# Kernel optimization log

Measured on AMD Instinct MI355X. Metric: run time of the kernel, lower is better.

The kernel has to match this reference:

```python
import jax, jax.numpy as jnp
import numpy as np
from jax import lax

SEQ, BATCH, INPUT, HIDDEN = 2048, 32, 256, 256


def setup_inputs() -> dict:
    key = jax.random.key(0)
    k1, k2, k3 = jax.random.split(key, 3)
    scale = 1.0 / np.sqrt(HIDDEN)
    return {
        "input": jax.random.normal(k1, (SEQ, BATCH, INPUT), dtype=jnp.float32),
        "W_ih": jax.random.normal(k2, (3 * HIDDEN, INPUT), dtype=jnp.float32) * scale,
        "W_hh": jax.random.normal(k3, (3 * HIDDEN, HIDDEN), dtype=jnp.float32) * scale,
        "b_ih": jnp.zeros((3 * HIDDEN,), dtype=jnp.float32),
        "b_hh": jnp.zeros((3 * HIDDEN,), dtype=jnp.float32),
    }


def reference(input, W_ih, W_hh, b_ih, b_hh):
    """Single-layer unidirectional CustomGRU forward.

    Faithful to the torch module, including its quirk: the n-gate gets the
    W_hh_n @ h contribution twice (once un-gated via `gates`, once gated by r).
    Returns (output [S,B,H], h_n [1,B,H]).
    """
    H = W_hh.shape[0] // 3
    W_hn = W_hh[2 * H:]  # [H, H]
    # Precompute input projections for all timesteps (same math, batched GEMM).
    x_proj = jnp.einsum('sbi,gi->sbg', input, W_ih) + b_ih + b_hh  # [S,B,3H]

    def step(h, xp):
        gates = xp + h @ W_hh.T  # [B, 3H]
        r, z, n = jnp.split(gates, 3, axis=1)
        r = jax.nn.sigmoid(r)
        z = jax.nn.sigmoid(z)
        n = jnp.tanh(n + r * (h @ W_hn.T))
        h_new = (1.0 - z) * n + z * h
        return h_new, h_new

    h0 = jnp.zeros((input.shape[1], H), dtype=input.dtype)
    h_last, output = lax.scan(step, h0, x_proj)
    return output, h_last[None, :, :]
```

## Files before the change

### kernel.cpp

```cpp
#include <hip/hip_runtime.h>
#include <stdint.h>
#include <stddef.h>

#define S_LEN 2048
#define BATCH 32
#define NIN   256
#define NH    256
#define NG    768
#define GRUB  32
#define XPB   2048

typedef _Float16 half2_t __attribute__((ext_vector_type(2)));
typedef _Float16 half8_t __attribute__((ext_vector_type(8)));
typedef int      int16v  __attribute__((ext_vector_type(16)));
typedef int      int4v   __attribute__((ext_vector_type(4)));

#if __has_builtin(__builtin_amdgcn_exp2f)
#define EXP2F(x) __builtin_amdgcn_exp2f(x)
#else
#define EXP2F(x) exp2f(x)
#endif

static __device__ __forceinline__ float fdot2(half2_t a, half2_t b, float c) {
  return __builtin_amdgcn_fdot2(a, b, c, false);
}
static __device__ __forceinline__ half2_t pack2(float lo, float hi) {
  half2_t r; r[0] = (_Float16)lo; r[1] = (_Float16)hi; return r;
}
static __device__ __forceinline__ float sigmoid_fast(float x) {
  float e = EXP2F(-1.44269504088896340736f * x);
  return 1.0f / (1.0f + e);
}
static __device__ __forceinline__ float tanh_fast(float x) {
  float e = EXP2F(2.88539008177792681472f * x);
  return 1.0f - 2.0f / (1.0f + e);
}
static __device__ __forceinline__ float dpp_xor1(float v) {
  return __builtin_bit_cast(float,
    __builtin_amdgcn_mov_dpp(__builtin_bit_cast(int, v), 0xB1, 0xF, 0xF, true));
}
static __device__ __forceinline__ float dpp_xor2(float v) {
  return __builtin_bit_cast(float,
    __builtin_amdgcn_mov_dpp(__builtin_bit_cast(int, v), 0x4E, 0xF, 0xF, true));
}

static __device__ __forceinline__ int flags_all12(const int* p) {
  int4v a, b, c;
  asm volatile("global_load_dwordx4 %0, %3, off sc0 sc1\n"
               "global_load_dwordx4 %1, %4, off sc0 sc1\n"
               "global_load_dwordx4 %2, %5, off sc0 sc1\n"
               "s_waitcnt vmcnt(0)"
               : "=v"(a), "=v"(b), "=v"(c)
               : "v"(p), "v"(p + 4), "v"(p + 8)
               : "memory");
  int all = a.x & a.y & a.z & a.w;
  all &= b.x & b.y & b.z & b.w;
  all &= c.x & c.y & c.z & c.w;
  return all;
}
#define FLAGWAIT(BASEP) do {                                                  \
    while (!flags_all12(BASEP)) __builtin_amdgcn_s_sleep(16);                 \
  } while (0)

#define BH(x)    __builtin_bit_cast(half2_t, (x))
#define BW(W, e) __builtin_bit_cast(half2_t, (int)((W)[e]))

#define DOT6(q, U0, U1, U2, U3, U4, U5, o) do {                               \
    a0 = fdot2(BW(U0,(o)+0), BH(q.x), a0); a1 = fdot2(BW(U1,(o)+0), BH(q.x), a1);\
    a2 = fdot2(BW(U2,(o)+0), BH(q.x), a2); a3 = fdot2(BW(U3,(o)+0), BH(q.x), a3);\
    a4 = fdot2(BW(U4,(o)+0), BH(q.x), a4); a5 = fdot2(BW(U5,(o)+0), BH(q.x), a5);\
    a0 = fdot2(BW(U0,(o)+1), BH(q.y), a0); a1 = fdot2(BW(U1,(o)+1), BH(q.y), a1);\
    a2 = fdot2(BW(U2,(o)+1), BH(q.y), a2); a3 = fdot2(BW(U3,(o)+1), BH(q.y), a3);\
    a4 = fdot2(BW(U4,(o)+1), BH(q.y), a4); a5 = fdot2(BW(U5,(o)+1), BH(q.y), a5);\
    a0 = fdot2(BW(U0,(o)+2), BH(q.z), a0); a1 = fdot2(BW(U1,(o)+2), BH(q.z), a1);\
    a2 = fdot2(BW(U2,(o)+2), BH(q.z), a2); a3 = fdot2(BW(U3,(o)+2), BH(q.z), a3);\
    a4 = fdot2(BW(U4,(o)+2), BH(q.z), a4); a5 = fdot2(BW(U5,(o)+2), BH(q.z), a5);\
    a0 = fdot2(BW(U0,(o)+3), BH(q.w), a0); a1 = fdot2(BW(U1,(o)+3), BH(q.w), a1);\
    a2 = fdot2(BW(U2,(o)+3), BH(q.w), a2); a3 = fdot2(BW(U3,(o)+3), BH(q.w), a3);\
    a4 = fdot2(BW(U4,(o)+3), BH(q.w), a4); a5 = fdot2(BW(U5,(o)+3), BH(q.w), a5);\
  } while (0)

#define LDW(W, o) do {                                                        \
    int4 q0 = wsrc[(o) + 0], q1 = wsrc[(o) + 1];                              \
    int4 q2 = wsrc[(o) + 2], q3 = wsrc[(o) + 3];                              \
    W = (int16v){q0.x, q0.y, q0.z, q0.w, q1.x, q1.y, q1.z, q1.w,              \
                 q2.x, q2.y, q2.z, q2.w, q3.x, q3.y, q3.z, q3.w};             \
  } while (0)

#define LOADPIN_W(SRC) \
  int16v W0a, W0b, W1a, W1b, W2a, W2b, W3a, W3b, W4a, W4b, W5a, W5b;         \
  {                                                                           \
    const int4* wsrc = (const int4*)(SRC);                                    \
    LDW(W0a, 0);  LDW(W0b, 4);  LDW(W1a, 8);  LDW(W1b, 12);                   \
    LDW(W2a, 16); LDW(W2b, 20); LDW(W3a, 24); LDW(W3b, 28);                   \
    LDW(W4a, 32); LDW(W4b, 36); LDW(W5a, 40); LDW(W5b, 44);                   \
  }                                                                           \
  asm volatile("" : "+v"(W0a), "+v"(W0b), "+v"(W1a), "+v"(W1b),               \
                    "+v"(W2a), "+v"(W2b), "+v"(W3a), "+v"(W3b),               \
                    "+v"(W4a), "+v"(W4b), "+v"(W5a), "+v"(W5b));

#define DOT6x8() do {                                                         \
    DOT6(q0, W0a, W1a, W2a, W3a, W4a, W5a, 0);                                \
    DOT6(q1, W0a, W1a, W2a, W3a, W4a, W5a, 4);                                \
    DOT6(q2, W0a, W1a, W2a, W3a, W4a, W5a, 8);                                \
    DOT6(q3, W0a, W1a, W2a, W3a, W4a, W5a, 12);                               \
    DOT6(q4, W0b, W1b, W2b, W3b, W4b, W5b, 0);                                \
    DOT6(q5, W0b, W1b, W2b, W3b, W4b, W5b, 4);                                \
    DOT6(q6, W0b, W1b, W2b, W3b, W4b, W5b, 8);                                \
    DOT6(q7, W0b, W1b, W2b, W3b, W4b, W5b, 12);                               \
  } while (0)

#define QREDUCE(MVR, MVZ, MVN) do {                                           \
    float b0 = a0 + dpp_xor1(a0), b1 = a1 + dpp_xor1(a1);                     \
    float b2 = a2 + dpp_xor1(a2), b3 = a3 + dpp_xor1(a3);                     \
    float b4 = a4 + dpp_xor1(a4), b5 = a5 + dpp_xor1(a5);                     \
    float xr_ = jj ? b1 : b0, xz_ = jj ? b3 : b2, xn_ = jj ? b5 : b4;         \
    MVR = xr_ + dpp_xor2(xr_);                                                \
    MVZ = xz_ + dpp_xor2(xz_);                                                \
    MVN = xn_ + dpp_xor2(xn_);                                                \
  } while (0)

__global__ __launch_bounds__(256) void prep_in_kernel(const float* __restrict__ in,
                                                      _Float16* __restrict__ in16,
                                                      int* __restrict__ flags) {
  size_t v = (size_t)blockIdx.x * 256 + threadIdx.x;
  if (blockIdx.x < 9) {
    int i = blockIdx.x * 256 + threadIdx.x;
    if (i < XPB) flags[i] = 0;
    else if (i < XPB + 8) flags[i] = 1;
  }
  const float4* p4 = (const float4*)in;
  float4 a = p4[v * 2 + 0];
  float4 b = p4[v * 2 + 1];
  half8_t o;
  o[0] = (_Float16)a.x; o[1] = (_Float16)a.y; o[2] = (_Float16)a.z; o[3] = (_Float16)a.w;
  o[4] = (_Float16)b.x; o[5] = (_Float16)b.y; o[6] = (_Float16)b.z; o[7] = (_Float16)b.w;
  ((half8_t*)in16)[v] = o;
}

__global__ __launch_bounds__(256) void prep_w_kernel(const float* __restrict__ W_ih,
                                                     const float* __restrict__ W_hh,
                                                     const float* __restrict__ b_ih,
                                                     const float* __restrict__ b_hh,
                                                     half2_t* __restrict__ whh3,
                                                     half2_t* __restrict__ wih3,
                                                     float* __restrict__ bias) {
  int idx = blockIdx.x * 256 + threadIdx.x;
  if (idx < 128 * NG) {
    int tid = idx / 192;
    int r   = idx - tid * 192;
    int d   = r >> 5, kk = r & 31;
    int gate = d >> 1, jj = d & 1;
    int c  = tid & 3, j1 = tid >> 2;
    int row = gate * NH + 2 * j1 + jj;
    int col = 64 * c + 2 * kk;
    whh3[idx] = pack2(W_hh[(size_t)row * NH + col], W_hh[(size_t)row * NH + col + 1]);
  } else if (idx < 2 * 128 * NG) {
    int i2  = idx - 128 * NG;
    int tid = i2 / 192;
    int r   = i2 - tid * 192;
    int d   = r >> 5, kk = r & 31;
    int gate = d >> 1, jj = d & 1;
    int c  = tid & 3, j1 = tid >> 2;
    int row = gate * NH + 2 * j1 + jj;
    int col = 64 * c + 2 * kk;
    wih3[i2] = pack2(W_ih[(size_t)row * NIN + col], W_ih[(size_t)row * NIN + col + 1]);
  } else if (idx < 2 * 128 * NG + NG) {
    int g = idx - 2 * 128 * NG;
    bias[g] = b_ih[g] + b_hh[g];
  }
}

__global__
__attribute__((amdgpu_flat_work_group_size(512, 512), amdgpu_waves_per_eu(2, 2)))
void fused_kernel(const _Float16* __restrict__ in16,
                  const half2_t* __restrict__ wih3,
                  const float* __restrict__ bias,
                  float* __restrict__ xp,
                  const half2_t* __restrict__ whh3,
                  float* __restrict__ out,
                  int* __restrict__ flags) {
  const int tid = threadIdx.x;
  const int c   = tid & 3;
  const int j1  = tid >> 2;
  const int jj  = c & 1;
  const int jmine = 2 * j1 + jj;

  if (blockIdx.x >= GRUB) {
    const int xb = (int)blockIdx.x - GRUB;
    LOADPIN_W(wih3 + (size_t)tid * 192);
    const float bgr = bias[jmine], bgz = bias[NH + jmine], bgn = bias[2 * NH + jmine];
    const char* inrow = (const char*)(in16 + (size_t)xb * 32 * NIN) + c * 128;
    float* xo = xp + (size_t)xb * 32 * NG + jmine;
    for (int rr = 0; rr < 32; ++rr) {
      float a0 = 0.f, a1 = 0.f, a2 = 0.f, a3 = 0.f, a4 = 0.f, a5 = 0.f;
      int4 q0 = *(const int4*)(inrow +   0), q1 = *(const int4*)(inrow +  16);
      int4 q2 = *(const int4*)(inrow +  32), q3 = *(const int4*)(inrow +  48);
      int4 q4 = *(const int4*)(inrow +  64), q5 = *(const int4*)(inrow +  80);
      int4 q6 = *(const int4*)(inrow +  96), q7 = *(const int4*)(inrow + 112);
      DOT6x8();
      float mvr, mvz, mvn;
      QREDUCE(mvr, mvz, mvn);
      if (c < 2) {
        xo[0]      = mvr + bgr;
        xo[NH]     = mvz + bgz;
        xo[2 * NH] = mvn + bgn;
      }
      inrow += NIN * 2;
      xo += NG;
    }
    __syncthreads();
    if (tid == 0)
      __hip_atomic_store(&flags[xb], 1, __ATOMIC_RELEASE, __HIP_MEMORY_SCOPE_AGENT);
    return;
  }

  const int b = blockIdx.x;
  LOADPIN_W(whh3 + (size_t)tid * 192);

  __shared__ __attribute__((aligned(16))) char smh[1152];
  if (tid < 288) ((int*)smh)[tid] = 0;

  FLAGWAIT(flags);

  const float* xq = xp + (size_t)b * NG + jmine;
  float xr_c = xq[0], xz_c = xq[NH], xn_c = xq[2 * NH];
  xq += (size_t)BATCH * NG;
  float* op = out + (size_t)b * NH + jmine;

  const int wofs = 144 * (jmine >> 6) + 2 * (jmine & 63);

  float h = 0.f;
  __syncthreads();

#define GSTEP(RB, WB) do {                                                    \
    float xr_n = xq[0], xz_n = xq[NH], xn_n = xq[2 * NH];                     \
    const char* hb = smh + (RB) + c * 144;                                    \
    float a0 = 0.f, a1 = 0.f, a2 = 0.f, a3 = 0.f, a4 = 0.f, a5 = 0.f;        \
    int4 q0 = *(const int4*)(hb +   0), q1 = *(const int4*)(hb +  16);       \
    int4 q2 = *(const int4*)(hb +  32), q3 = *(const int4*)(hb +  48);       \
    int4 q4 = *(const int4*)(hb +  64), q5 = *(const int4*)(hb +  80);       \
    int4 q6 = *(const int4*)(hb +  96), q7 = *(const int4*)(hb + 112);       \
    DOT6x8();                                                                 \
    float mvr, mvz, mvn;                                                      \
    QREDUCE(mvr, mvz, mvn);                                                   \
    float r = sigmoid_fast(xr_c + mvr);                                       \
    float z = sigmoid_fast(xz_c + mvz);                                       \
    float n = tanh_fast(xn_c + mvn + r * mvn);              \
    h = z * (h - n) + n;                                                      \
    if (c < 2) {                                                              \
      op[0] = h;                                                              \
      *(_Float16*)(smh + (WB) + wofs) = (_Float16)h;                          \
    }                                                                         \
    asm volatile("s_waitcnt lgkmcnt(0)\n\ts_barrier" ::: "memory");           \
    xr_c = xr_n; xz_c = xz_n; xn_c = xn_n;                                    \
    xq += (size_t)BATCH * NG;                                                 \
    op += (size_t)BATCH * NH;                                                 \
  } while (0)

  for (int t0 = 0; t0 < S_LEN; t0 += 8) {
    if (t0) FLAGWAIT(flags + t0);
    for (int u = 0; u < 4; ++u) {
      GSTEP(0, 576);
      GSTEP(576, 0);
    }
  }
#undef GSTEP

  if (c < 2) out[(size_t)S_LEN * BATCH * NH + (size_t)b * NH + jmine] = h;
}

extern "C" void kernel_launch(void* const* d_in, const int* in_sizes, int n_in,
                              void* d_out, int out_size, void* d_ws, size_t ws_size,
                              hipStream_t stream) {
  const float* input = (const float*)d_in[0];
  const float* W_ih  = (const float*)d_in[1];
  const float* W_hh  = (const float*)d_in[2];
  const float* b_ih  = (const float*)d_in[3];
  const float* b_hh  = (const float*)d_in[4];
  float* out = (float*)d_out;

  const size_t SB = (size_t)S_LEN * BATCH;
  const size_t xp_b   = SB * NG * 4;
  const size_t in16_b = SB * NIN * 2;
  const size_t w_b    = (size_t)128 * NG * 4;

  char* p = (char*)d_ws;
  float*    xp    = (float*)p;                p += xp_b;
  _Float16* in16  = (_Float16*)p;             p += in16_b;
  half2_t*  whh3  = (half2_t*)p;              p += w_b;
  half2_t*  wih3  = (half2_t*)p;              p += w_b;
  float*    bias  = (float*)p;                p += (size_t)NG * 4;
  uintptr_t fp_ = (((uintptr_t)p) + 127) & ~(uintptr_t)127;
  int*      flags = (int*)fp_;

  prep_in_kernel<<<8192, 256, 0, stream>>>(input, in16, flags);
  prep_w_kernel<<<(2 * 128 * NG + NG + 255) / 256, 256, 0, stream>>>(W_ih, W_hh, b_ih, b_hh,
                                                                     whh3, wih3, bias);
  fused_kernel<<<GRUB + XPB, 512, 0, stream>>>(in16, wih3, bias, xp, whh3, out, flags);
  (void)out_size; (void)n_in; (void)in_sizes; (void)ws_size;
}
```

Baseline: 2.362 ms.

## Fuse input fp16 conversion into projection blocks and coarsen flag polling

Drops the separate prep_in kernel that converted the whole input to fp16. The projection blocks now read fp32 input directly and pack it to half2 in registers, and flag initialisation moves into the weight-prep kernel. The recurrent blocks now poll 36 flags once every 32 timesteps instead of 12 flags every 8. This removes a full pass over the input and one launch, and cuts how often the recurrence polls. In exchange the projection blocks read twice as many input bytes, and the recurrence may stall longer waiting for a larger chunk of projections to be ready.

New measurement: 2.349 ms. About the same (-0.6%).

```diff
diff --git a/kernel.cpp b/kernel.cpp
--- a/kernel.cpp
+++ b/kernel.cpp
@@ -11,7 +11,6 @@
 #define XPB   2048
 
 typedef _Float16 half2_t __attribute__((ext_vector_type(2)));
-typedef _Float16 half8_t __attribute__((ext_vector_type(8)));
 typedef int      int16v  __attribute__((ext_vector_type(16)));
 typedef int      int4v   __attribute__((ext_vector_type(4)));
 
@@ -44,26 +43,40 @@
     __builtin_amdgcn_mov_dpp(__builtin_bit_cast(int, v), 0x4E, 0xF, 0xF, true));
 }
 
-static __device__ __forceinline__ int flags_all12(const int* p) {
-  int4v a, b, c;
-  asm volatile("global_load_dwordx4 %0, %3, off sc0 sc1\n"
-               "global_load_dwordx4 %1, %4, off sc0 sc1\n"
-               "global_load_dwordx4 %2, %5, off sc0 sc1\n"
+static __device__ __forceinline__ int flags_all36(const int* p) {
+  int4v a0, a1, a2, a3, a4, a5, a6, a7, a8;
+  asm volatile("global_load_dwordx4 %0, %9, off sc0 sc1\n"
+               "global_load_dwordx4 %1, %9, off offset:16 sc0 sc1\n"
+               "global_load_dwordx4 %2, %9, off offset:32 sc0 sc1\n"
+               "global_load_dwordx4 %3, %9, off offset:48 sc0 sc1\n"
+               "global_load_dwordx4 %4, %9, off offset:64 sc0 sc1\n"
+               "global_load_dwordx4 %5, %9, off offset:80 sc0 sc1\n"
+               "global_load_dwordx4 %6, %9, off offset:96 sc0 sc1\n"
+               "global_load_dwordx4 %7, %9, off offset:112 sc0 sc1\n"
+               "global_load_dwordx4 %8, %9, off offset:128 sc0 sc1\n"
                "s_waitcnt vmcnt(0)"
-               : "=v"(a), "=v"(b), "=v"(c)
-               : "v"(p), "v"(p + 4), "v"(p + 8)
+               : "=v"(a0), "=v"(a1), "=v"(a2), "=v"(a3), "=v"(a4),
+                 "=v"(a5), "=v"(a6), "=v"(a7), "=v"(a8)
+               : "v"(p)
                : "memory");
-  int all = a.x & a.y & a.z & a.w;
-  all &= b.x & b.y & b.z & b.w;
-  all &= c.x & c.y & c.z & c.w;
+  int all = a0.x & a0.y & a0.z & a0.w;
+  all &= a1.x & a1.y & a1.z & a1.w;
+  all &= a2.x & a2.y & a2.z & a2.w;
+  all &= a3.x & a3.y & a3.z & a3.w;
+  all &= a4.x & a4.y & a4.z & a4.w;
+  all &= a5.x & a5.y & a5.z & a5.w;
+  all &= a6.x & a6.y & a6.z & a6.w;
+  all &= a7.x & a7.y & a7.z & a7.w;
+  all &= a8.x & a8.y & a8.z & a8.w;
   return all;
 }
-#define FLAGWAIT(BASEP) do {                                                  \
-    while (!flags_all12(BASEP)) __builtin_amdgcn_s_sleep(16);                 \
+#define FLAGWAIT36(BASEP) do {                                                \
+    while (!flags_all36(BASEP)) __builtin_amdgcn_s_sleep(16);                 \
   } while (0)
 
 #define BH(x)    __builtin_bit_cast(half2_t, (x))
 #define BW(W, e) __builtin_bit_cast(half2_t, (int)((W)[e]))
+#define P2I(a, b) __builtin_bit_cast(int, pack2((a), (b)))
 
 #define DOT6(q, U0, U1, U2, U3, U4, U5, o) do {                               \
     a0 = fdot2(BW(U0,(o)+0), BH(q.x), a0); a1 = fdot2(BW(U1,(o)+0), BH(q.x), a1);\
@@ -120,31 +133,14 @@
     MVN = xn_ + dpp_xor2(xn_);                                                \
   } while (0)
 
-__global__ __launch_bounds__(256) void prep_in_kernel(const float* __restrict__ in,
-                                                      _Float16* __restrict__ in16,
-                                                      int* __restrict__ flags) {
-  size_t v = (size_t)blockIdx.x * 256 + threadIdx.x;
-  if (blockIdx.x < 9) {
-    int i = blockIdx.x * 256 + threadIdx.x;
-    if (i < XPB) flags[i] = 0;
-    else if (i < XPB + 8) flags[i] = 1;
-  }
-  const float4* p4 = (const float4*)in;
-  float4 a = p4[v * 2 + 0];
-  float4 b = p4[v * 2 + 1];
-  half8_t o;
-  o[0] = (_Float16)a.x; o[1] = (_Float16)a.y; o[2] = (_Float16)a.z; o[3] = (_Float16)a.w;
-  o[4] = (_Float16)b.x; o[5] = (_Float16)b.y; o[6] = (_Float16)b.z; o[7] = (_Float16)b.w;
-  ((half8_t*)in16)[v] = o;
-}
-
 __global__ __launch_bounds__(256) void prep_w_kernel(const float* __restrict__ W_ih,
                                                      const float* __restrict__ W_hh,
                                                      const float* __restrict__ b_ih,
                                                      const float* __restrict__ b_hh,
                                                      half2_t* __restrict__ whh3,
                                                      half2_t* __restrict__ wih3,
-                                                     float* __restrict__ bias) {
+                                                     float* __restrict__ bias,
+                                                     int* __restrict__ flags) {
   int idx = blockIdx.x * 256 + threadIdx.x;
   if (idx < 128 * NG) {
     int tid = idx / 192;
@@ -168,12 +164,15 @@
   } else if (idx < 2 * 128 * NG + NG) {
     int g = idx - 2 * 128 * NG;
     bias[g] = b_ih[g] + b_hh[g];
+  } else if (idx < 2 * 128 * NG + NG + XPB + 16) {
+    int k = idx - (2 * 128 * NG + NG);
+    flags[k] = (k < XPB) ? 0 : 1;
   }
 }
 
 __global__
 __attribute__((amdgpu_flat_work_group_size(512, 512), amdgpu_waves_per_eu(2, 2)))
-void fused_kernel(const _Float16* __restrict__ in16,
+void fused_kernel(const float* __restrict__ inf,
                   const half2_t* __restrict__ wih3,
                   const float* __restrict__ bias,
                   float* __restrict__ xp,
@@ -190,15 +189,25 @@
     const int xb = (int)blockIdx.x - GRUB;
     LOADPIN_W(wih3 + (size_t)tid * 192);
     const float bgr = bias[jmine], bgz = bias[NH + jmine], bgn = bias[2 * NH + jmine];
-    const char* inrow = (const char*)(in16 + (size_t)xb * 32 * NIN) + c * 128;
+    const float4* fr = (const float4*)(inf + (size_t)xb * 32 * NIN + c * 64);
     float* xo = xp + (size_t)xb * 32 * NG + jmine;
     for (int rr = 0; rr < 32; ++rr) {
       float a0 = 0.f, a1 = 0.f, a2 = 0.f, a3 = 0.f, a4 = 0.f, a5 = 0.f;
-      int4 q0 = *(const int4*)(inrow +   0), q1 = *(const int4*)(inrow +  16);
-      int4 q2 = *(const int4*)(inrow +  32), q3 = *(const int4*)(inrow +  48);
-      int4 q4 = *(const int4*)(inrow +  64), q5 = *(const int4*)(inrow +  80);
-      int4 q6 = *(const int4*)(inrow +  96), q7 = *(const int4*)(inrow + 112);
-      DOT6x8();
+      float4 g0, g1; int4 q;
+#define XB(IDX, U0, U1, U2, U3, U4, U5, OFF)                                  \
+      g0 = fr[2 * (IDX)]; g1 = fr[2 * (IDX) + 1];                             \
+      q.x = P2I(g0.x, g0.y); q.y = P2I(g0.z, g0.w);                           \
+      q.z = P2I(g1.x, g1.y); q.w = P2I(g1.z, g1.w);                           \
+      DOT6(q, U0, U1, U2, U3, U4, U5, OFF);
+      XB(0, W0a, W1a, W2a, W3a, W4a, W5a, 0)
+      XB(1, W0a, W1a, W2a, W3a, W4a, W5a, 4)
+      XB(2, W0a, W1a, W2a, W3a, W4a, W5a, 8)
+      XB(3, W0a, W1a, W2a, W3a, W4a, W5a, 12)
+      XB(4, W0b, W1b, W2b, W3b, W4b, W5b, 0)
+      XB(5, W0b, W1b, W2b, W3b, W4b, W5b, 4)
+      XB(6, W0b, W1b, W2b, W3b, W4b, W5b, 8)
+      XB(7, W0b, W1b, W2b, W3b, W4b, W5b, 12)
+#undef XB
       float mvr, mvz, mvn;
       QREDUCE(mvr, mvz, mvn);
       if (c < 2) {
@@ -206,7 +215,7 @@
         xo[NH]     = mvz + bgz;
         xo[2 * NH] = mvn + bgn;
       }
-      inrow += NIN * 2;
+      fr += 64;
       xo += NG;
     }
     __syncthreads();
@@ -221,7 +230,7 @@
   __shared__ __attribute__((aligned(16))) char smh[1152];
   if (tid < 288) ((int*)smh)[tid] = 0;
 
-  FLAGWAIT(flags);
+  FLAGWAIT36(flags);
 
   const float* xq = xp + (size_t)b * NG + jmine;
   float xr_c = xq[0], xz_c = xq[NH], xn_c = xq[2 * NH];
@@ -259,7 +268,7 @@
   } while (0)
 
   for (int t0 = 0; t0 < S_LEN; t0 += 8) {
-    if (t0) FLAGWAIT(flags + t0);
+    if (t0 && (t0 & 31) == 0) FLAGWAIT36(flags + t0);
     for (int u = 0; u < 4; ++u) {
       GSTEP(0, 576);
       GSTEP(576, 0);
@@ -281,22 +290,20 @@
   float* out = (float*)d_out;
 
   const size_t SB = (size_t)S_LEN * BATCH;
-  const size_t xp_b   = SB * NG * 4;
-  const size_t in16_b = SB * NIN * 2;
-  const size_t w_b    = (size_t)128 * NG * 4;
+  const size_t xp_b = SB * NG * 4;
+  const size_t w_b  = (size_t)128 * NG * 4;
 
   char* p = (char*)d_ws;
   float*    xp    = (float*)p;                p += xp_b;
-  _Float16* in16  = (_Float16*)p;             p += in16_b;
   half2_t*  whh3  = (half2_t*)p;              p += w_b;
   half2_t*  wih3  = (half2_t*)p;              p += w_b;
   float*    bias  = (float*)p;                p += (size_t)NG * 4;
   uintptr_t fp_ = (((uintptr_t)p) + 127) & ~(uintptr_t)127;
   int*      flags = (int*)fp_;
 
-  prep_in_kernel<<<8192, 256, 0, stream>>>(input, in16, flags);
-  prep_w_kernel<<<(2 * 128 * NG + NG + 255) / 256, 256, 0, stream>>>(W_ih, W_hh, b_ih, b_hh,
-                                                                     whh3, wih3, bias);
-  fused_kernel<<<GRUB + XPB, 512, 0, stream>>>(in16, wih3, bias, xp, whh3, out, flags);
+  const int prep_items = 2 * 128 * NG + NG + XPB + 16;
+  prep_w_kernel<<<(prep_items + 255) / 256, 256, 0, stream>>>(W_ih, W_hh, b_ih, b_hh,
+                                                              whh3, wih3, bias, flags);
+  fused_kernel<<<GRUB + XPB, 512, 0, stream>>>(input, wih3, bias, xp, whh3, out, flags);
   (void)out_size; (void)n_in; (void)in_sizes; (void)ws_size;
 }
```
